# Kernel optimization log

Hardware: AMD Instinct MI355X
Metric: run time of the kernel (lower is better)

Reference implementation:

```python
import jax, jax.numpy as jnp
import numpy as np

D_MODEL = 1024
N_HEADS = 16
WINDOW = 256
CAUSAL = True


def build_sliding_window_mask(T, window_size, causal=True):
    half = window_size // 2
    i = jnp.arange(T)[:, None]
    j = jnp.arange(T)[None, :]
    attend = jnp.abs(i - j) <= half
    if causal:
        attend = attend & (j <= i)
    return jnp.where(attend, 0.0, -jnp.inf).astype(jnp.float32)  # (T, T)


def setup_inputs() -> dict:
    key = jax.random.key(0)
    kx, kq, kk, kv, ko = jax.random.split(key, 5)
    B, T, D = 2, 2048, D_MODEL
    s = 1.0 / np.sqrt(D)
    return {
        "x": jax.random.normal(kx, (B, T, D), jnp.float32),
        "Wq": jax.random.normal(kq, (D, D), jnp.float32) * s,
        "Wk": jax.random.normal(kk, (D, D), jnp.float32) * s,
        "Wv": jax.random.normal(kv, (D, D), jnp.float32) * s,
        "Wo": jax.random.normal(ko, (D, D), jnp.float32) * s,
    }


def reference(x, Wq, Wk, Wv, Wo):
    B, T, D = x.shape
    H = N_HEADS
    dh = D // H
    # torch nn.Linear: y = x @ W.T
    def proj(W):
        return (x @ W.T).reshape(B, T, H, dh).transpose(0, 2, 1, 3)  # (B,H,T,dh)

    q, k, v = proj(Wq), proj(Wk), proj(Wv)
    scale = jnp.sqrt(jnp.asarray(dh, x.dtype))
    scores = jnp.einsum("bhtd,bhsd->bhts", q, k) / scale  # (B,H,T,T)
    mask = build_sliding_window_mask(T, WINDOW, CAUSAL)
    scores = scores + mask[None, None]
    attn = jax.nn.softmax(scores, axis=-1)
    attn = jnp.nan_to_num(attn, nan=0.0)
    out = jnp.einsum("bhts,bhsd->bhtd", attn, v)  # (B,H,T,dh)
    out = out.transpose(0, 2, 1, 3).reshape(B, T, D)
    return out @ Wo.T
```

## Files before the change

### kernel.cpp

```cpp
#include <hip/hip_runtime.h>
#include <hip/hip_bf16.h>

#define B_  2
#define T_  2048
#define D_  1024
#define H_  16
#define DH_ 64
#define M_  (B_ * T_)

typedef short s16x8 __attribute__((ext_vector_type(8)));
typedef float f32x4 __attribute__((ext_vector_type(4)));

__device__ inline float bfu(unsigned short u) {
    union { unsigned int i; float f; } c; c.i = ((unsigned int)u) << 16; return c.f;
}
__device__ inline unsigned short f2bf(float f) {
    union { float f; unsigned int i; } c; c.f = f;
    unsigned int r = c.i + 0x7fffu + ((c.i >> 16) & 1u);
    return (unsigned short)(r >> 16);
}
__device__ inline void stv(float* p, float v) { *p = v; }
__device__ inline void stv(unsigned short* p, float v) { *p = f2bf(v); }

__device__ inline void gload_lds16(const unsigned short* g, unsigned short* l) {
    __builtin_amdgcn_global_load_lds(
        (const __attribute__((address_space(1))) void*)g,
        (__attribute__((address_space(3))) void*)l, 16, 0, 0);
}

__global__ __launch_bounds__(256) void conv_bf16(const float* __restrict__ x,
                                                 const float* __restrict__ Wq,
                                                 const float* __restrict__ Wk,
                                                 const float* __restrict__ Wv,
                                                 const float* __restrict__ Wo,
                                                 unsigned short* __restrict__ dst) {
    const int g = blockIdx.x * 256 + threadIdx.x;
    const float* s; size_t o;
    if (g < (1 << 20)) { s = x; o = (size_t)g; }
    else {
        int gg = g - (1 << 20);
        int w = gg >> 18;
        o = (size_t)(gg & ((1 << 18) - 1));
        s = (w == 0) ? Wq : (w == 1) ? Wk : (w == 2) ? Wv : Wo;
    }
    float4 v = ((const float4*)s)[o];
    ushort4 u;
    u.x = f2bf(v.x); u.y = f2bf(v.y); u.z = f2bf(v.z); u.w = f2bf(v.w);
    ((ushort4*)dst)[g] = u;
}

template <int BM, typename Tout>
__global__ __launch_bounds__(256) void gemm_m97(const unsigned short* __restrict__ A,
                                                const unsigned short* __restrict__ Bw,
                                                Tout* __restrict__ C0,
                                                Tout* __restrict__ C1,
                                                unsigned short* __restrict__ vtr,
                                                int K) {
    constexpr int MI = BM / 32;
    __shared__ unsigned short As[2 * BM * 32];
    __shared__ unsigned short Bs[2 * 128 * 32];
    const int tid  = threadIdx.x;
    const int lane = tid & 63;
    const int wave = tid >> 6;
    const int wr = wave >> 1, wc = wave & 1;
    const int bm = blockIdx.y * BM, bn = blockIdx.x * 128;
    const int fr = lane & 15, kg = lane >> 4;
    const int lrow = lane >> 2;
    const int lcol = (lane & 3) * 8;

    f32x4 acc[MI][4];
    #pragma unroll
    for (int mi = 0; mi < MI; ++mi)
        #pragma unroll
        for (int ni = 0; ni < 4; ++ni)
            #pragma unroll
            for (int r = 0; r < 4; ++r) acc[mi][ni][r] = 0.f;

    const unsigned short* ga = A  + (size_t)(bm + wave * 16 + lrow) * K + lcol;
    const unsigned short* gb = Bw + (size_t)(bn + wave * 16 + lrow) * K + lcol;
    unsigned short* la = &As[(wave * 16) * 32];
    unsigned short* lb = &Bs[(wave * 16) * 32];

    for (int k0 = 0; k0 < K; k0 += 64) {
        __syncthreads();
        #pragma unroll
        for (int hf = 0; hf < 2; ++hf) {
            #pragma unroll
            for (int s = 0; s < BM / 64; ++s)
                gload_lds16(ga + k0 + hf * 32 + (size_t)(s * 64) * K,
                            la + hf * BM * 32 + s * 64 * 32);
            gload_lds16(gb + k0 + hf * 32,                  lb + hf * 128 * 32);
            gload_lds16(gb + k0 + hf * 32 + (size_t)64 * K, lb + hf * 128 * 32 + 64 * 32);
        }
        __syncthreads();
        #pragma unroll
        for (int hf = 0; hf < 2; ++hf) {
            s16x8 af[MI], bfv[4];
            #pragma unroll
            for (int mi = 0; mi < MI; ++mi)
                af[mi] = *(const s16x8*)&As[hf * BM * 32 + (wr * (BM / 2) + mi * 16 + fr) * 32 + kg * 8];
            #pragma unroll
            for (int ni = 0; ni < 4; ++ni)
                bfv[ni] = *(const s16x8*)&Bs[hf * 128 * 32 + (wc * 64 + ni * 16 + fr) * 32 + kg * 8];
            #pragma unroll
            for (int mi = 0; mi < MI; ++mi)
                #pragma unroll
                for (int ni = 0; ni < 4; ++ni)
                    acc[mi][ni] = __builtin_amdgcn_mfma_f32_16x16x32_bf16(af[mi], bfv[ni], acc[mi][ni], 0, 0, 0);
        }
    }

    if (vtr && bn >= 2048) {
        #pragma unroll
        for (int mi = 0; mi < MI; ++mi)
            #pragma unroll
            for (int ni = 0; ni < 4; ++ni) {
                const int nl = (bn - 2048) + wc * 64 + ni * 16 + fr;
                const int h = nl >> 6, d = nl & 63;
                const int m0 = bm + wr * (BM / 2) + mi * 16 + kg * 4;
                const int b = m0 >> 11, t0 = m0 & (T_ - 1);
                ushort4 u;
                u.x = f2bf(acc[mi][ni][0]); u.y = f2bf(acc[mi][ni][1]);
                u.z = f2bf(acc[mi][ni][2]); u.w = f2bf(acc[mi][ni][3]);
                *(ushort4*)(vtr + ((size_t)(b * H_ + h) * 64 + d) * T_ + t0) = u;
            }
        return;
    }
    Tout* C = (bn < 1024) ? C0 : C1;
    const int nb = bn & 1023;
    #pragma unroll
    for (int mi = 0; mi < MI; ++mi)
        #pragma unroll
        for (int ni = 0; ni < 4; ++ni)
            #pragma unroll
            for (int r = 0; r < 4; ++r) {
                int m = bm + wr * (BM / 2) + mi * 16 + kg * 4 + r;
                int n = nb + wc * 64 + ni * 16 + fr;
                stv(&C[(size_t)m * 1024 + n], acc[mi][ni][r]);
            }
}

__global__ __launch_bounds__(256) void swa_mfma2(const unsigned short* qb,
                                                 const unsigned short* __restrict__ kb,
                                                 const unsigned short* __restrict__ vt,
                                                 unsigned short* ob) {
    __shared__ unsigned short Ks[192 * 64];
    __shared__ unsigned short Pl[4][16 * 168];
    const int wave = threadIdx.x >> 6;
    const int lane = threadIdx.x & 63;
    const int blk = blockIdx.x;
    const int i0b = (blk & 31) * 64;
    const int bh  = blk >> 5;
    const int h = bh & (H_ - 1), b = bh >> 4;
    const int g = lane >> 4, l15 = lane & 15;

    const size_t rowbase = (size_t)b * T_ * D_ + (size_t)h * DH_;
    const int klo2 = (i0b > 128) ? (i0b - 128) : 0;

    {
        const unsigned short* kg0 = kb + rowbase
            + (size_t)(klo2 + (lane >> 3)) * D_ + (lane & 7) * 8;
        #pragma unroll
        for (int s = 0; s < 6; ++s) {
            const int i = wave * 6 + s;
            gload_lds16(kg0 + (size_t)(i * 8) * D_, &Ks[i * 8 * 64]);
        }
    }

    const int i0  = i0b + wave * 16;
    const int klo = (i0 > 128) ? (i0 - 128) : 0;
    const int koff = klo - klo2;

    unsigned short* Pw = Pl[wave];
    {
        int row = lane >> 2, col = 144 + (lane & 3) * 4;
        *(uint2*)&Pw[row * 168 + col] = make_uint2(0u, 0u);
    }

    const unsigned short* qrow = qb + rowbase + (size_t)(i0 + l15) * D_ + g * 8;
    const s16x8 aq0 = *(const s16x8*)(qrow);
    const s16x8 aq1 = *(const s16x8*)(qrow + 32);

    __syncthreads();

    f32x4 sacc[9];
    #pragma unroll
    for (int t = 0; t < 9; ++t)
        #pragma unroll
        for (int r = 0; r < 4; ++r) sacc[t][r] = 0.f;

    #pragma unroll
    for (int t = 0; t < 9; ++t) {
        const unsigned short* kr = &Ks[(koff + t * 16 + l15) * 64 + g * 8];
        s16x8 b0 = *(const s16x8*)kr;
        s16x8 b1 = *(const s16x8*)(kr + 32);
        sacc[t] = __builtin_amdgcn_mfma_f32_16x16x32_bf16(aq0, b0, sacc[t], 0, 0, 0);
        sacc[t] = __builtin_amdgcn_mfma_f32_16x16x32_bf16(aq1, b1, sacc[t], 0, 0, 0);
    }

    float mrow[4] = {-1e30f, -1e30f, -1e30f, -1e30f};
    #pragma unroll
    for (int t = 0; t < 9; ++t)
        #pragma unroll
        for (int r = 0; r < 4; ++r) {
            const int j  = klo + t * 16 + l15;
            const int iq = i0 + g * 4 + r;
            const bool valid = (j <= iq) && (j + 128 >= iq);
            const float s = valid ? sacc[t][r] * 0.125f : -1e30f;
            sacc[t][r] = s;
            mrow[r] = fmaxf(mrow[r], s);
        }
    #pragma unroll
    for (int r = 0; r < 4; ++r)
        #pragma unroll
        for (int off = 1; off < 16; off <<= 1)
            mrow[r] = fmaxf(mrow[r], __shfl_xor(mrow[r], off));

    float lrow[4] = {0.f, 0.f, 0.f, 0.f};
    #pragma unroll
    for (int t = 0; t < 9; ++t)
        #pragma unroll
        for (int r = 0; r < 4; ++r) {
            const float p = __expf(sacc[t][r] - mrow[r]);
            sacc[t][r] = p;
            lrow[r] += p;
        }
    #pragma unroll
    for (int r = 0; r < 4; ++r) {
        #pragma unroll
        for (int off = 1; off < 16; off <<= 1)
            lrow[r] += __shfl_xor(lrow[r], off);
    }
    float invl[4];
    #pragma unroll
    for (int r = 0; r < 4; ++r) invl[r] = 1.f / lrow[r];

    #pragma unroll
    for (int t = 0; t < 9; ++t)
        #pragma unroll
        for (int r = 0; r < 4; ++r)
            Pw[(g * 4 + r) * 168 + t * 16 + l15] = f2bf(sacc[t][r]);

    f32x4 oacc[4];
    #pragma unroll
    for (int nt = 0; nt < 4; ++nt)
        #pragma unroll
        for (int r = 0; r < 4; ++r) oacc[nt][r] = 0.f;

    const unsigned short* vtb = vt + (size_t)bh * 64 * T_;
    #pragma unroll
    for (int kt = 0; kt < 5; ++kt) {
        const s16x8 ap = *(const s16x8*)&Pw[l15 * 168 + kt * 32 + g * 8];
        #pragma unroll
        for (int nt = 0; nt < 4; ++nt) {
            const unsigned short* vrow = vtb + (size_t)(nt * 16 + l15) * T_ + klo + kt * 32 + g * 8;
            s16x8 bv = *(const s16x8*)vrow;
            oacc[nt] = __builtin_amdgcn_mfma_f32_16x16x32_bf16(ap, bv, oacc[nt], 0, 0, 0);
        }
    }

    #pragma unroll
    for (int nt = 0; nt < 4; ++nt)
        #pragma unroll
        for (int r = 0; r < 4; ++r) {
            const float val = oacc[nt][r] * invl[r];
            ob[rowbase + (size_t)(i0 + g * 4 + r) * D_ + nt * 16 + l15] = f2bf(val);
        }
}

extern "C" void kernel_launch(void* const* d_in, const int* in_sizes, int n_in,
                              void* d_out, int out_size, void* d_ws, size_t ws_size,
                              hipStream_t stream) {
    const float* x  = (const float*)d_in[0];
    const float* Wq = (const float*)d_in[1];
    const float* Wk = (const float*)d_in[2];
    const float* Wv = (const float*)d_in[3];
    const float* Wo = (const float*)d_in[4];

    const size_t MD = (size_t)M_ * D_;
    const size_t WN = (size_t)D_ * D_;

    unsigned short* wsb = (unsigned short*)d_ws;
    unsigned short* xb  = wsb;
    unsigned short* Wqb = xb + MD;
    unsigned short* Wob = Wqb + 3 * WN;
    unsigned short* qb  = Wob + WN;
    unsigned short* vt = (unsigned short*)d_out;
    unsigned short* kb = vt + MD;

    conv_bf16<<<8192, 256, 0, stream>>>(x, Wq, Wk, Wv, Wo, wsb);

    gemm_m97<128, unsigned short><<<dim3(24, M_ / 128), 256, 0, stream>>>(
        xb, Wqb, qb, kb, vt, D_);

    swa_mfma2<<<(B_ * H_ * T_) / 64, 256, 0, stream>>>(qb, kb, vt, qb);

    gemm_m97<64, float><<<dim3(8, M_ / 64), 256, 0, stream>>>(
        qb, Wob, (float*)d_out, (float*)d_out, nullptr, D_);
}
```

Measured before the change: 156.4 us.

## Stage V tiles in swizzled LDS, swizzle K layout, deepen output GEMM k-step

The attention kernel now loads the V^T window into shared memory once per block with an XOR swizzle, instead of each wave reading V directly from global memory. The K tile in shared memory gets an XOR swizzle to avoid bank conflicts on the MFMA operand reads. The output-projection GEMM is templated to load four 32-wide K slices per synchronisation instead of two, halving its barrier count at the cost of more LDS per block. The extra V buffer raises LDS use in the attention kernel, which could lower occupancy.

```diff
diff --git a/kernel.cpp b/kernel.cpp
--- a/kernel.cpp
+++ b/kernel.cpp
@@ -49,7 +49,7 @@
     ((ushort4*)dst)[g] = u;
 }
 
-template <int BM, typename Tout>
+template <int BM, int NH, typename Tout>
 __global__ __launch_bounds__(256) void gemm_m97(const unsigned short* __restrict__ A,
                                                 const unsigned short* __restrict__ Bw,
                                                 Tout* __restrict__ C0,
@@ -57,8 +57,8 @@
                                                 unsigned short* __restrict__ vtr,
                                                 int K) {
     constexpr int MI = BM / 32;
-    __shared__ unsigned short As[2 * BM * 32];
-    __shared__ unsigned short Bs[2 * 128 * 32];
+    __shared__ unsigned short As[NH * BM * 32];
+    __shared__ unsigned short Bs[NH * 128 * 32];
     const int tid  = threadIdx.x;
     const int lane = tid & 63;
     const int wave = tid >> 6;
@@ -81,10 +81,10 @@
     unsigned short* la = &As[(wave * 16) * 32];
     unsigned short* lb = &Bs[(wave * 16) * 32];
 
-    for (int k0 = 0; k0 < K; k0 += 64) {
+    for (int k0 = 0; k0 < K; k0 += 32 * NH) {
         __syncthreads();
         #pragma unroll
-        for (int hf = 0; hf < 2; ++hf) {
+        for (int hf = 0; hf < NH; ++hf) {
             #pragma unroll
             for (int s = 0; s < BM / 64; ++s)
                 gload_lds16(ga + k0 + hf * 32 + (size_t)(s * 64) * K,
@@ -94,7 +94,7 @@
         }
         __syncthreads();
         #pragma unroll
-        for (int hf = 0; hf < 2; ++hf) {
+        for (int hf = 0; hf < NH; ++hf) {
             s16x8 af[MI], bfv[4];
             #pragma unroll
             for (int mi = 0; mi < MI; ++mi)
@@ -140,11 +140,12 @@
             }
 }
 
-__global__ __launch_bounds__(256) void swa_mfma2(const unsigned short* qb,
+__global__ __launch_bounds__(256) void swa_mfma3(const unsigned short* qb,
                                                  const unsigned short* __restrict__ kb,
                                                  const unsigned short* __restrict__ vt,
                                                  unsigned short* ob) {
     __shared__ unsigned short Ks[192 * 64];
+    __shared__ unsigned short Vs[64 * 208];
     __shared__ unsigned short Pl[4][16 * 168];
     const int wave = threadIdx.x >> 6;
     const int lane = threadIdx.x & 63;
@@ -158,12 +159,27 @@
     const int klo2 = (i0b > 128) ? (i0b - 128) : 0;
 
     {
-        const unsigned short* kg0 = kb + rowbase
-            + (size_t)(klo2 + (lane >> 3)) * D_ + (lane & 7) * 8;
+        const int lr = lane >> 3;
+        const int gc = (lane & 7) ^ lr;
+        const unsigned short* kg0 = kb + rowbase + (size_t)(klo2 + lr) * D_ + gc * 8;
         #pragma unroll
         for (int s = 0; s < 6; ++s) {
             const int i = wave * 6 + s;
             gload_lds16(kg0 + (size_t)(i * 8) * D_, &Ks[i * 8 * 64]);
+        }
+    }
+    {
+        const unsigned short* vtb = vt + (size_t)bh * 64 * T_ + klo2;
+        #pragma unroll
+        for (int s = 0; s < 7; ++s) {
+            const int i = s * 4 + wave;
+            if (i < 26) {
+                const int cc = i * 64 + lane;
+                const int d  = cc / 26;
+                const int sl = cc - d * 26;
+                const int c  = (sl < 24) ? (sl ^ (d & 7)) : sl;
+                gload_lds16(vtb + (size_t)d * T_ + c * 8, &Vs[i * 512]);
+            }
         }
     }
 
@@ -191,9 +207,10 @@
 
     #pragma unroll
     for (int t = 0; t < 9; ++t) {
-        const unsigned short* kr = &Ks[(koff + t * 16 + l15) * 64 + g * 8];
-        s16x8 b0 = *(const s16x8*)kr;
-        s16x8 b1 = *(const s16x8*)(kr + 32);
+        const int row = koff + t * 16 + l15;
+        const int r7 = row & 7;
+        s16x8 b0 = *(const s16x8*)&Ks[row * 64 + ((g     ^ r7) * 8)];
+        s16x8 b1 = *(const s16x8*)&Ks[row * 64 + (((g+4) ^ r7) * 8)];
         sacc[t] = __builtin_amdgcn_mfma_f32_16x16x32_bf16(aq0, b0, sacc[t], 0, 0, 0);
         sacc[t] = __builtin_amdgcn_mfma_f32_16x16x32_bf16(aq1, b1, sacc[t], 0, 0, 0);
     }
@@ -247,14 +264,16 @@
         #pragma unroll
         for (int r = 0; r < 4; ++r) oacc[nt][r] = 0.f;
 
-    const unsigned short* vtb = vt + (size_t)bh * 64 * T_;
+    const int kc0 = koff >> 3;
     #pragma unroll
     for (int kt = 0; kt < 5; ++kt) {
         const s16x8 ap = *(const s16x8*)&Pw[l15 * 168 + kt * 32 + g * 8];
         #pragma unroll
         for (int nt = 0; nt < 4; ++nt) {
-            const unsigned short* vrow = vtb + (size_t)(nt * 16 + l15) * T_ + klo + kt * 32 + g * 8;
-            s16x8 bv = *(const s16x8*)vrow;
+            const int d = nt * 16 + l15;
+            const int c = kc0 + kt * 4 + g;
+            const int sl = (c < 24) ? (c ^ (d & 7)) : c;
+            s16x8 bv = *(const s16x8*)&Vs[d * 208 + sl * 8];
             oacc[nt] = __builtin_amdgcn_mfma_f32_16x16x32_bf16(ap, bv, oacc[nt], 0, 0, 0);
         }
     }
@@ -290,11 +309,11 @@
 
     conv_bf16<<<8192, 256, 0, stream>>>(x, Wq, Wk, Wv, Wo, wsb);
 
-    gemm_m97<128, unsigned short><<<dim3(24, M_ / 128), 256, 0, stream>>>(
+    gemm_m97<128, 2, unsigned short><<<dim3(24, M_ / 128), 256, 0, stream>>>(
         xb, Wqb, qb, kb, vt, D_);
 
-    swa_mfma2<<<(B_ * H_ * T_) / 64, 256, 0, stream>>>(qb, kb, vt, qb);
-
-    gemm_m97<64, float><<<dim3(8, M_ / 64), 256, 0, stream>>>(
+    swa_mfma3<<<(B_ * H_ * T_) / 64, 256, 0, stream>>>(qb, kb, vt, qb);
+
+    gemm_m97<64, 4, float><<<dim3(8, M_ / 64), 256, 0, stream>>>(
         qb, Wob, (float*)d_out, (float*)d_out, nullptr, D_);
 }
```

Result: faster. 149.4 us (-4.5%).
